# Kernel tuning notes

Hardware: AMD Instinct MI355X
Metric: run time of the kernel (lower is better)

The kernel has to match this reference:

```python
import jax, jax.numpy as jnp
import numpy as np


def setup_inputs() -> dict:
    key = jax.random.key(0)
    k = jax.random.split(key, 6)
    N, Cin, H, W = 16, 256, 14, 14   # ROI mask features
    D = 256                          # dim_reduced
    C = 20                           # number of FALKON classifiers (num_classes - 1)
    M = 512                          # max Nystrom centers (padded)
    x = jax.random.normal(k[0], (N, Cin, H, W), jnp.float32)
    # torch ConvTranspose2d weight layout: [in, out, kH, kW]
    conv_w = jax.random.normal(k[1], (Cin, D, 2, 2), jnp.float32) * 0.05
    conv_b = jnp.zeros((D,), jnp.float32)
    mean = jax.random.normal(k[2], (D,), jnp.float32) * 0.1
    mean_norm = jnp.full((1,), 10.0, jnp.float32)
    ny = jax.random.normal(k[3], (C, M, D), jnp.float32)
    alpha = jax.random.normal(k[4], (C, M, 1), jnp.float32) * 0.01
    sigma = jnp.full((1,), 25.0, jnp.float32)
    return {"x": x, "conv_w": conv_w, "conv_b": conv_b, "mean": mean,
            "mean_norm": mean_norm, "ny": ny, "alpha": alpha, "sigma": sigma}


def reference(x, conv_w, conv_b, mean, mean_norm, ny, alpha, sigma):
    N, Cin, H, W = x.shape
    D = conv_w.shape[1]
    C = ny.shape[0]
    # ConvTranspose2d(kernel=2, stride=2, pad=0): each input pixel expands to a 2x2 block.
    y = jnp.einsum('nchw,coij->nohiwj', x, conv_w).reshape(N, D, 2 * H, 2 * W)
    y = jax.nn.relu(y + conv_b[None, :, None, None])
    fw = y.shape[2]                                   # feat_width = 28
    # permute(0,2,3,1).reshape(-1, D): pixel order (roi, h, w)
    f = y.transpose(0, 2, 3, 1).reshape(-1, D)        # [P, D], P = N*fw*fw
    f = (f - mean) * (20.0 / mean_norm[0])
    # Batched Gaussian kernel mmv: K[c,p,m] = exp(-||f_p - ny_cm||^2 / (2 sigma^2))
    sq = (jnp.sum(f * f, axis=-1)[None, :, None]
          + jnp.sum(ny * ny, axis=-1)[:, None, :]
          - 2.0 * jnp.einsum('pd,cmd->cpm', f, ny))   # [C, P, M]
    K = jnp.exp(-sq / (2.0 * sigma[0] ** 2))
    scores = jnp.einsum('cpm,cm->cp', K, alpha[..., 0])  # [C, P]
    P = f.shape[0]
    bg = jnp.full((P, 1), -2.0, f.dtype)              # background column of -2
    ps = jnp.concatenate([bg, scores.T], axis=1)      # [P, C+1]
    # per-ROI: [fw*fw, C+1].T.reshape(C+1, fw, fw) == reshape(N, fw, fw, C+1) -> NCHW
    out = ps.reshape(N, fw, fw, C + 1).transpose(0, 3, 1, 2)
    return out
```

## Files before the change

kernel.cpp:

```cpp
#include <hip/hip_runtime.h>

typedef __bf16 bf16_t;
typedef __bf16 bf16x8 __attribute__((ext_vector_type(8)));
typedef __bf16 bf16x4 __attribute__((ext_vector_type(4)));
typedef float  f32x4  __attribute__((ext_vector_type(4)));
typedef float  f32x16 __attribute__((ext_vector_type(16)));
typedef char   i8x16  __attribute__((ext_vector_type(16)));
typedef char   i8x4   __attribute__((ext_vector_type(4)));
typedef int    i32x4  __attribute__((ext_vector_type(4)));

#define PIX 196
#define P_  12544
#define M_  512
#define SF  12.0f
#define SN  24.0f

__device__ inline void gload_lds16(const void* g, void* l) {
  __builtin_amdgcn_global_load_lds((const __attribute__((address_space(1))) void*)g,
                                   (__attribute__((address_space(3))) void*)l,
                                   16, 0, 0);
}

__global__ __launch_bounds__(256) void k_prep(const float* __restrict__ conv_w,
                                              const float* __restrict__ x,
                                              const float* __restrict__ ny,
                                              const float* __restrict__ alpha,
                                              const float* __restrict__ sigma,
                                              bf16_t* __restrict__ wtb,
                                              bf16_t* __restrict__ xb,
                                              char* __restrict__ nys8,
                                              float* __restrict__ e_n) {
  __shared__ float xs[16][198];
  int bid = blockIdx.x, tid = threadIdx.x;
  if (bid < 2560) {
    int l = tid & 63;
    int row = bid * 4 + (tid >> 6);
    int c = row >> 9, m = row & 511;
    f32x4 v = *reinterpret_cast<const f32x4*>(ny + row * 256 + l * 4);
    i8x4 q8;
    float sq = 0.f;
#pragma unroll
    for (int i = 0; i < 4; ++i) {
      float fq = fminf(fmaxf(__builtin_rintf(v[i] * SN), -127.f), 127.f);
      q8[i] = (char)(int)fq;
      float fv = fq * (1.f / SN);
      sq += fv * fv;
    }
    int u = m >> 5, mf = (m >> 4) & 1, mc = m & 15;
    int ks = l >> 4, lg = (l >> 2) & 3, j0 = (l & 3) * 4;
    *reinterpret_cast<i8x4*>(nys8 + (c * 16 + u) * 8192 + mf * 4096 + ks * 1024 +
                             (lg * 16 + mc) * 16 + j0) = q8;
#pragma unroll
    for (int o = 1; o < 64; o <<= 1) sq += __shfl_xor(sq, o);
    if (l == 0) {
      float s = sigma[0];
      e_n[row] = __expf(-sq / (2.f * s * s)) * alpha[row];
    }
  } else if (bid < 2816) {
    int c = bid - 2560, d = tid;
    f32x4 w = *reinterpret_cast<const f32x4*>(conv_w + (c * 256 + d) * 4);
    int ks = c >> 4, kb = (c >> 3) & 1, j = c & 7;
#pragma unroll
    for (int q = 0; q < 4; ++q) {
      int col = q * 256 + d;
      int cf = col >> 5;
      int lfrag = kb * 32 + (col & 31);
      wtb[((cf * 16 + ks) * 64 + lfrag) * 8 + j] = (bf16_t)w[q];
    }
  } else {
    int idx2 = bid - 2816;
    int n = idx2 >> 4, c0 = (idx2 & 15) * 16;
    const float* xp = x + (n * 256 + c0) * PIX;
#pragma unroll
    for (int r = 0; r < 13; ++r) {
      int idx = r * 256 + tid;
      if (idx < 3136) xs[idx / PIX][idx % PIX] = xp[idx];
    }
    __syncthreads();
#pragma unroll
    for (int r = 0; r < 4; ++r) {
      int idx = r * 256 + tid;
      if (idx < 784) {
        int hw = idx >> 2, c4 = idx & 3;
        bf16x4 h;
#pragma unroll
        for (int i = 0; i < 4; ++i) h[i] = (bf16_t)xs[c4 * 4 + i][hw];
        *reinterpret_cast<bf16x4*>(xb + (n * PIX + hw) * 256 + c0 + c4 * 4) = h;
      }
    }
  }
}

__global__ __launch_bounds__(256) void k_convT(const bf16_t* __restrict__ xb,
                                               const bf16_t* __restrict__ wtb,
                                               const float* __restrict__ conv_b,
                                               const float* __restrict__ mean,
                                               const float* __restrict__ mean_norm,
                                               char* __restrict__ fb8) {
  __shared__ bf16_t bs[32768];
  int rb = blockIdx.x * 64, cbase = blockIdx.y * 128;
  int tid = threadIdx.x, w = tid >> 6, l = tid & 63;
  int wr = w >> 1, wc = w & 1;
  const bf16_t* bsrc = wtb + blockIdx.y * 32768;
#pragma unroll
  for (int r = 0; r < 16; ++r) {
    int s = (r * 4 + w) * 64 + l;
    gload_lds16(bsrc + s * 8, bs + s * 8);
  }
  bf16x8 a[16];
  {
    const bf16_t* ap = xb + (rb + wr * 32 + (l & 31)) * 256 + (l >> 5) * 8;
#pragma unroll
    for (int ks = 0; ks < 16; ++ks) a[ks] = *reinterpret_cast<const bf16x8*>(ap + ks * 16);
  }
  __syncthreads();
  float scale = (20.f / mean_norm[0]) * SF;
  int hi = l >> 5;
#pragma unroll
  for (int cf = 0; cf < 2; ++cf) {
    f32x16 acc = {0.f,0.f,0.f,0.f,0.f,0.f,0.f,0.f,0.f,0.f,0.f,0.f,0.f,0.f,0.f,0.f};
#pragma unroll
    for (int ks = 0; ks < 16; ++ks) {
      bf16x8 b = *reinterpret_cast<const bf16x8*>(bs + ((wc * 2 + cf) * 16 + ks) * 512 + l * 8);
      acc = __builtin_amdgcn_mfma_f32_32x32x16_bf16(a[ks], b, acc, 0, 0, 0);
    }
    int col = cbase + wc * 64 + cf * 32 + (l & 31);
    int q = col >> 8, d = col & 255;
    float bias = conv_b[d], mn = mean[d];
    int qi = q >> 1, qj = q & 1;
#pragma unroll
    for (int r = 0; r < 16; ++r) {
      int p3 = rb + wr * 32 + (r & 3) + 8 * (r >> 2) + 4 * hi;
      int n = p3 / PIX, hw = p3 % PIX;
      int h = hw / 14, ww = hw % 14;
      int p = n * 784 + (2 * h + qi) * 28 + 2 * ww + qj;
      float v = fmaxf(acc[r] + bias, 0.f);
      float fq = fminf(fmaxf(__builtin_rintf((v - mn) * scale), -127.f), 127.f);
      fb8[p * 256 + d] = (char)(int)fq;
    }
  }
}

__global__ __launch_bounds__(256, 4) void k_falkon(const char* __restrict__ fb8,
                                                   const char* __restrict__ nys8,
                                                   const float* __restrict__ e_n,
                                                   const float* __restrict__ sigma,
                                                   float* __restrict__ out) {
  __shared__ char bs[2][8192];
  __shared__ float lds_en[512];
  int c = blockIdx.y, pb = blockIdx.x * 128;
  int tid = threadIdx.x, w = tid >> 6, l = tid & 63;

  if (c == 0 && tid < 128) {
    int p = pb + tid;
    out[(p / 784) * 16464 + (p % 784)] = -2.0f;
  }

  lds_en[tid] = e_n[c * M_ + tid];
  lds_en[256 + tid] = e_n[c * M_ + 256 + tid];

  i32x4 a[2][4];
  {
    const char* ap = fb8 + (pb + w * 32 + (l & 15)) * 256 + (l >> 4) * 16;
#pragma unroll
    for (int rf = 0; rf < 2; ++rf)
#pragma unroll
      for (int ks = 0; ks < 4; ++ks)
        a[rf][ks] = *reinterpret_cast<const i32x4*>(ap + rf * 16 * 256 + ks * 64);
  }

  float sg = sigma[0];
  float kl = 1.44269504088896340736f / (sg * sg);
  float Ksc = kl * (1.f / (SF * SN));

  float ef0, ef1;
#pragma unroll
  for (int rf = 0; rf < 2; ++rf) {
    int ssi = 0;
#pragma unroll
    for (int ks = 0; ks < 4; ++ks) {
      i8x16 q = __builtin_bit_cast(i8x16, a[rf][ks]);
#pragma unroll
      for (int j = 0; j < 16; ++j) {
        int qv = (signed char)q[j];
        ssi += qv * qv;
      }
    }
    ssi += __shfl_xor(ssi, 16);
    ssi += __shfl_xor(ssi, 32);
    float ef = __builtin_amdgcn_exp2f(-(float)ssi * (0.5f * kl / (SF * SF)));
    if (rf == 0) ef0 = ef; else ef1 = ef;
  }

  f32x4 sacc[2];
  sacc[0] = {0.f, 0.f, 0.f, 0.f};
  sacc[1] = {0.f, 0.f, 0.f, 0.f};

  const char* nb = nys8 + c * (16 * 8192);

  auto stage = [&](int u) {
    const char* src = nb + u * 8192;
    char* dst = &bs[u & 1][0];
#pragma unroll
    for (int r = 0; r < 2; ++r) {
      int slot = r * 256 + tid;
      gload_lds16(src + slot * 16, dst + slot * 16);
    }
  };

  stage(0);
  stage(1);
  asm volatile("s_waitcnt vmcnt(2) lgkmcnt(0)" ::: "memory");
  __builtin_amdgcn_s_barrier();

  for (int u = 0; u < 16; ++u) {
    const char* bp = &bs[u & 1][0] + l * 16;
    i32x4 b[2][4];
#pragma unroll
    for (int mf = 0; mf < 2; ++mf)
#pragma unroll
      for (int ks = 0; ks < 4; ++ks)
        b[mf][ks] = *reinterpret_cast<const i32x4*>(bp + mf * 4096 + ks * 1024);

    i32x4 acc[2][2];
#pragma unroll
    for (int rf = 0; rf < 2; ++rf)
#pragma unroll
      for (int mf = 0; mf < 2; ++mf) acc[rf][mf] = {0, 0, 0, 0};

    __builtin_amdgcn_s_setprio(1);
#pragma unroll
    for (int ks = 0; ks < 4; ++ks)
#pragma unroll
      for (int rf = 0; rf < 2; ++rf)
#pragma unroll
        for (int mf = 0; mf < 2; ++mf)
          acc[rf][mf] = __builtin_amdgcn_mfma_i32_16x16x64_i8(a[rf][ks], b[mf][ks],
                                                              acc[rf][mf], 0, 0, 0);
    __builtin_amdgcn_s_setprio(0);

    float en0 = lds_en[u * 32 + (l & 15)];
    float en1 = lds_en[u * 32 + 16 + (l & 15)];
#pragma unroll
    for (int rf = 0; rf < 2; ++rf)
#pragma unroll
      for (int r = 0; r < 4; ++r) {
        sacc[rf][r] += en0 * __builtin_amdgcn_exp2f((float)acc[rf][0][r] * Ksc)
                     + en1 * __builtin_amdgcn_exp2f((float)acc[rf][1][r] * Ksc);
      }

    if (u < 15) {
      asm volatile("s_waitcnt lgkmcnt(0)" ::: "memory");
      __builtin_amdgcn_s_barrier();
      if (u + 2 < 16) {
        stage(u + 2);
        asm volatile("s_waitcnt vmcnt(2)" ::: "memory");
      } else {
        asm volatile("s_waitcnt vmcnt(0)" ::: "memory");
      }
      __builtin_amdgcn_s_barrier();
    }
  }

#pragma unroll
  for (int rf = 0; rf < 2; ++rf)
#pragma unroll
    for (int r = 0; r < 4; ++r) {
      float v = sacc[rf][r];
      v += __shfl_xor(v, 1);
      v += __shfl_xor(v, 2);
      v += __shfl_xor(v, 4);
      v += __shfl_xor(v, 8);
      int rr = (l >> 4) * 4 + r;
      float ef = __shfl(rf == 0 ? ef0 : ef1, rr);
      if ((l & 15) == 0) {
        int p = pb + w * 32 + rf * 16 + rr;
        out[(p / 784) * 16464 + (c + 1) * 784 + (p % 784)] = v * ef;
      }
    }
}

extern "C" void kernel_launch(void* const* d_in, const int* in_sizes, int n_in,
                              void* d_out, int out_size, void* d_ws, size_t ws_size,
                              hipStream_t stream) {
  const float* x         = (const float*)d_in[0];
  const float* conv_w    = (const float*)d_in[1];
  const float* conv_b    = (const float*)d_in[2];
  const float* mean      = (const float*)d_in[3];
  const float* mean_norm = (const float*)d_in[4];
  const float* ny        = (const float*)d_in[5];
  const float* alpha     = (const float*)d_in[6];
  const float* sigma     = (const float*)d_in[7];
  float* out = (float*)d_out;

  char* ws = (char*)d_ws;
  bf16_t* wtb  = (bf16_t*)ws;
  bf16_t* xb   = (bf16_t*)(ws + 524288);
  char*   fb8  = (char*)(ws + 2129920);
  char*   nys8 = (char*)(ws + 5341184);
  float*  e_n  = (float*)(ws + 7962624);

  k_prep<<<dim3(3072), dim3(256), 0, stream>>>(conv_w, x, ny, alpha, sigma,
                                               wtb, xb, nys8, e_n);
  k_convT<<<dim3(49, 8), dim3(256), 0, stream>>>(xb, wtb, conv_b, mean, mean_norm, fb8);
  k_falkon<<<dim3(98, 20), dim3(256), 0, stream>>>(fb8, nys8, e_n, sigma, out);
}
```

Measured before the change: 66.17 us.

## Software-pipeline MFMA of next tile with exp epilogue of previous tile

```diff
diff --git a/kernel.cpp b/kernel.cpp
--- a/kernel.cpp
+++ b/kernel.cpp
@@ -141,7 +141,7 @@
   }
 }
 
-__global__ __launch_bounds__(256, 4) void k_falkon(const char* __restrict__ fb8,
+__global__ __launch_bounds__(256, 3) void k_falkon(const char* __restrict__ fb8,
                                                    const char* __restrict__ nys8,
                                                    const float* __restrict__ e_n,
                                                    const float* __restrict__ sigma,
@@ -208,58 +208,82 @@
     }
   };
 
+  i32x4 bA[2][4], bB[2][4], accA[2][2], accB[2][2];
+
+  auto loadB0 = [&](i32x4 (&b)[2][4]) {
+    const char* bp = &bs[0][0] + l * 16;
+#pragma unroll
+    for (int mf = 0; mf < 2; ++mf)
+#pragma unroll
+      for (int ks = 0; ks < 4; ++ks)
+        b[mf][ks] = *reinterpret_cast<const i32x4*>(bp + mf * 4096 + ks * 1024);
+  };
+  auto loadB1 = [&](i32x4 (&b)[2][4]) {
+    const char* bp = &bs[1][0] + l * 16;
+#pragma unroll
+    for (int mf = 0; mf < 2; ++mf)
+#pragma unroll
+      for (int ks = 0; ks < 4; ++ks)
+        b[mf][ks] = *reinterpret_cast<const i32x4*>(bp + mf * 4096 + ks * 1024);
+  };
+  auto mfmaC = [&](const i32x4 (&b)[2][4], i32x4 (&acc)[2][2]) {
+#pragma unroll
+    for (int rf = 0; rf < 2; ++rf)
+#pragma unroll
+      for (int mf = 0; mf < 2; ++mf) acc[rf][mf] = {0, 0, 0, 0};
+    __builtin_amdgcn_s_setprio(1);
+#pragma unroll
+    for (int ks = 0; ks < 4; ++ks)
+#pragma unroll
+      for (int rf = 0; rf < 2; ++rf)
+#pragma unroll
+        for (int mf = 0; mf < 2; ++mf)
+          acc[rf][mf] = __builtin_amdgcn_mfma_i32_16x16x64_i8(a[rf][ks], b[mf][ks],
+                                                              acc[rf][mf], 0, 0, 0);
+    __builtin_amdgcn_s_setprio(0);
+  };
+  auto expS = [&](int u, const i32x4 (&acc)[2][2]) {
+    float en0 = lds_en[u * 32 + (l & 15)];
+    float en1 = lds_en[u * 32 + 16 + (l & 15)];
+#pragma unroll
+    for (int rf = 0; rf < 2; ++rf)
+#pragma unroll
+      for (int r = 0; r < 4; ++r) {
+        sacc[rf][r] += en0 * __builtin_amdgcn_exp2f((float)acc[rf][0][r] * Ksc)
+                     + en1 * __builtin_amdgcn_exp2f((float)acc[rf][1][r] * Ksc);
+      }
+  };
+  auto handoff = [&](int u) {
+    asm volatile("s_waitcnt lgkmcnt(0)" ::: "memory");
+    __builtin_amdgcn_s_barrier();
+    if (u + 2 < 16) {
+      stage(u + 2);
+      asm volatile("s_waitcnt vmcnt(2)" ::: "memory");
+    } else {
+      asm volatile("s_waitcnt vmcnt(0)" ::: "memory");
+    }
+    __builtin_amdgcn_s_barrier();
+  };
+
   stage(0);
   stage(1);
   asm volatile("s_waitcnt vmcnt(2) lgkmcnt(0)" ::: "memory");
   __builtin_amdgcn_s_barrier();
 
-  for (int u = 0; u < 16; ++u) {
-    const char* bp = &bs[u & 1][0] + l * 16;
-    i32x4 b[2][4];
-#pragma unroll
-    for (int mf = 0; mf < 2; ++mf)
-#pragma unroll
-      for (int ks = 0; ks < 4; ++ks)
-        b[mf][ks] = *reinterpret_cast<const i32x4*>(bp + mf * 4096 + ks * 1024);
-
-    i32x4 acc[2][2];
-#pragma unroll
-    for (int rf = 0; rf < 2; ++rf)
-#pragma unroll
-      for (int mf = 0; mf < 2; ++mf) acc[rf][mf] = {0, 0, 0, 0};
-
-    __builtin_amdgcn_s_setprio(1);
-#pragma unroll
-    for (int ks = 0; ks < 4; ++ks)
-#pragma unroll
-      for (int rf = 0; rf < 2; ++rf)
-#pragma unroll
-        for (int mf = 0; mf < 2; ++mf)
-          acc[rf][mf] = __builtin_amdgcn_mfma_i32_16x16x64_i8(a[rf][ks], b[mf][ks],
-                                                              acc[rf][mf], 0, 0, 0);
-    __builtin_amdgcn_s_setprio(0);
-
-    float en0 = lds_en[u * 32 + (l & 15)];
-    float en1 = lds_en[u * 32 + 16 + (l & 15)];
-#pragma unroll
-    for (int rf = 0; rf < 2; ++rf)
-#pragma unroll
-      for (int r = 0; r < 4; ++r) {
-        sacc[rf][r] += en0 * __builtin_amdgcn_exp2f((float)acc[rf][0][r] * Ksc)
-                     + en1 * __builtin_amdgcn_exp2f((float)acc[rf][1][r] * Ksc);
-      }
-
-    if (u < 15) {
-      asm volatile("s_waitcnt lgkmcnt(0)" ::: "memory");
-      __builtin_amdgcn_s_barrier();
-      if (u + 2 < 16) {
-        stage(u + 2);
-        asm volatile("s_waitcnt vmcnt(2)" ::: "memory");
-      } else {
-        asm volatile("s_waitcnt vmcnt(0)" ::: "memory");
-      }
-      __builtin_amdgcn_s_barrier();
-    }
+  loadB0(bA);
+  mfmaC(bA, accA);
+  for (int t = 0; t < 8; ++t) {
+    int u = 2 * t;
+    handoff(u);
+    loadB1(bB);
+    mfmaC(bB, accB);
+    expS(u, accA);
+    if (u + 2 < 16) {
+      handoff(u + 1);
+      loadB0(bA);
+      mfmaC(bA, accA);
+    }
+    expS(u + 1, accB);
   }
 
 #pragma unroll
```

Result: slower. 70.54 us (+6.6%).

## Split Nystrom centers across waves with per-wave staging and LDS reduction

Applied to the files above, without the earlier changes.

```diff
diff --git a/kernel.cpp b/kernel.cpp
--- a/kernel.cpp
+++ b/kernel.cpp
@@ -141,17 +141,19 @@
   }
 }
 
-__global__ __launch_bounds__(256, 4) void k_falkon(const char* __restrict__ fb8,
+__global__ __launch_bounds__(256, 2) void k_falkon(const char* __restrict__ fb8,
                                                    const char* __restrict__ nys8,
                                                    const float* __restrict__ e_n,
                                                    const float* __restrict__ sigma,
                                                    float* __restrict__ out) {
-  __shared__ char bs[2][8192];
+  __shared__ char bs[4][2][8192];
   __shared__ float lds_en[512];
-  int c = blockIdx.y, pb = blockIdx.x * 128;
+  __shared__ float part[4][64];
+  __shared__ float ef_l[64];
+  int c = blockIdx.y, pb = blockIdx.x * 64;
   int tid = threadIdx.x, w = tid >> 6, l = tid & 63;
 
-  if (c == 0 && tid < 128) {
+  if (c == 0 && tid < 64) {
     int p = pb + tid;
     out[(p / 784) * 16464 + (p % 784)] = -2.0f;
   }
@@ -159,11 +161,11 @@
   lds_en[tid] = e_n[c * M_ + tid];
   lds_en[256 + tid] = e_n[c * M_ + 256 + tid];
 
-  i32x4 a[2][4];
+  i32x4 a[4][4];
   {
-    const char* ap = fb8 + (pb + w * 32 + (l & 15)) * 256 + (l >> 4) * 16;
-#pragma unroll
-    for (int rf = 0; rf < 2; ++rf)
+    const char* ap = fb8 + (pb + (l & 15)) * 256 + (l >> 4) * 16;
+#pragma unroll
+    for (int rf = 0; rf < 4; ++rf)
 #pragma unroll
       for (int ks = 0; ks < 4; ++ks)
         a[rf][ks] = *reinterpret_cast<const i32x4*>(ap + rf * 16 * 256 + ks * 64);
@@ -173,9 +175,8 @@
   float kl = 1.44269504088896340736f / (sg * sg);
   float Ksc = kl * (1.f / (SF * SN));
 
-  float ef0, ef1;
-#pragma unroll
-  for (int rf = 0; rf < 2; ++rf) {
+#pragma unroll
+  for (int rf = 0; rf < 4; ++rf) {
     int ssi = 0;
 #pragma unroll
     for (int ks = 0; ks < 4; ++ks) {
@@ -188,43 +189,42 @@
     }
     ssi += __shfl_xor(ssi, 16);
     ssi += __shfl_xor(ssi, 32);
-    float ef = __builtin_amdgcn_exp2f(-(float)ssi * (0.5f * kl / (SF * SF)));
-    if (rf == 0) ef0 = ef; else ef1 = ef;
-  }
-
-  f32x4 sacc[2];
-  sacc[0] = {0.f, 0.f, 0.f, 0.f};
-  sacc[1] = {0.f, 0.f, 0.f, 0.f};
-
-  const char* nb = nys8 + c * (16 * 8192);
+    if (w == 0 && l < 16)
+      ef_l[rf * 16 + l] = __builtin_amdgcn_exp2f(-(float)ssi * (0.5f * kl / (SF * SF)));
+  }
+
+  f32x4 sacc[4];
+#pragma unroll
+  for (int rf = 0; rf < 4; ++rf) sacc[rf] = {0.f, 0.f, 0.f, 0.f};
+
+  const char* nb = nys8 + (c * 16 + w * 4) * 8192;
 
   auto stage = [&](int u) {
     const char* src = nb + u * 8192;
-    char* dst = &bs[u & 1][0];
-#pragma unroll
-    for (int r = 0; r < 2; ++r) {
-      int slot = r * 256 + tid;
-      gload_lds16(src + slot * 16, dst + slot * 16);
-    }
+    char* dst = &bs[w][u & 1][0];
+#pragma unroll
+    for (int r = 0; r < 8; ++r)
+      gload_lds16(src + (r * 64 + l) * 16, dst + (r * 64 + l) * 16);
   };
 
   stage(0);
   stage(1);
-  asm volatile("s_waitcnt vmcnt(2) lgkmcnt(0)" ::: "memory");
-  __builtin_amdgcn_s_barrier();
-
-  for (int u = 0; u < 16; ++u) {
-    const char* bp = &bs[u & 1][0] + l * 16;
+  __syncthreads();
+
+  for (int u = 0; u < 4; ++u) {
+    const char* bp = &bs[w][u & 1][0] + l * 16;
     i32x4 b[2][4];
 #pragma unroll
     for (int mf = 0; mf < 2; ++mf)
 #pragma unroll
       for (int ks = 0; ks < 4; ++ks)
         b[mf][ks] = *reinterpret_cast<const i32x4*>(bp + mf * 4096 + ks * 1024);
-
-    i32x4 acc[2][2];
-#pragma unroll
-    for (int rf = 0; rf < 2; ++rf)
+    asm volatile("s_waitcnt lgkmcnt(0)" ::: "memory");
+    if (u + 2 < 4) stage(u + 2);
+
+    i32x4 acc[4][2];
+#pragma unroll
+    for (int rf = 0; rf < 4; ++rf)
 #pragma unroll
       for (int mf = 0; mf < 2; ++mf) acc[rf][mf] = {0, 0, 0, 0};
 
@@ -232,38 +232,32 @@
 #pragma unroll
     for (int ks = 0; ks < 4; ++ks)
 #pragma unroll
-      for (int rf = 0; rf < 2; ++rf)
+      for (int rf = 0; rf < 4; ++rf)
 #pragma unroll
         for (int mf = 0; mf < 2; ++mf)
           acc[rf][mf] = __builtin_amdgcn_mfma_i32_16x16x64_i8(a[rf][ks], b[mf][ks],
                                                               acc[rf][mf], 0, 0, 0);
     __builtin_amdgcn_s_setprio(0);
 
-    float en0 = lds_en[u * 32 + (l & 15)];
-    float en1 = lds_en[u * 32 + 16 + (l & 15)];
-#pragma unroll
-    for (int rf = 0; rf < 2; ++rf)
+    float en0 = lds_en[w * 128 + u * 32 + (l & 15)];
+    float en1 = lds_en[w * 128 + u * 32 + 16 + (l & 15)];
+#pragma unroll
+    for (int rf = 0; rf < 4; ++rf)
 #pragma unroll
       for (int r = 0; r < 4; ++r) {
         sacc[rf][r] += en0 * __builtin_amdgcn_exp2f((float)acc[rf][0][r] * Ksc)
                      + en1 * __builtin_amdgcn_exp2f((float)acc[rf][1][r] * Ksc);
       }
 
-    if (u < 15) {
-      asm volatile("s_waitcnt lgkmcnt(0)" ::: "memory");
-      __builtin_amdgcn_s_barrier();
-      if (u + 2 < 16) {
-        stage(u + 2);
-        asm volatile("s_waitcnt vmcnt(2)" ::: "memory");
-      } else {
-        asm volatile("s_waitcnt vmcnt(0)" ::: "memory");
-      }
-      __builtin_amdgcn_s_barrier();
-    }
-  }
-
-#pragma unroll
-  for (int rf = 0; rf < 2; ++rf)
+    if (u == 1) {
+      asm volatile("s_waitcnt vmcnt(8)" ::: "memory");
+    } else if (u == 2) {
+      asm volatile("s_waitcnt vmcnt(0)" ::: "memory");
+    }
+  }
+
+#pragma unroll
+  for (int rf = 0; rf < 4; ++rf)
 #pragma unroll
     for (int r = 0; r < 4; ++r) {
       float v = sacc[rf][r];
@@ -271,13 +265,15 @@
       v += __shfl_xor(v, 2);
       v += __shfl_xor(v, 4);
       v += __shfl_xor(v, 8);
-      int rr = (l >> 4) * 4 + r;
-      float ef = __shfl(rf == 0 ? ef0 : ef1, rr);
-      if ((l & 15) == 0) {
-        int p = pb + w * 32 + rf * 16 + rr;
-        out[(p / 784) * 16464 + (c + 1) * 784 + (p % 784)] = v * ef;
-      }
-    }
+      if ((l & 15) == 0) part[w][rf * 16 + (l >> 4) * 4 + r] = v;
+    }
+  __syncthreads();
+
+  if (tid < 64) {
+    float s = part[0][tid] + part[1][tid] + part[2][tid] + part[3][tid];
+    int p = pb + tid;
+    out[(p / 784) * 16464 + (c + 1) * 784 + (p % 784)] = s * ef_l[tid];
+  }
 }
 
 extern "C" void kernel_launch(void* const* d_in, const int* in_sizes, int n_in,
@@ -303,5 +299,5 @@
   k_prep<<<dim3(3072), dim3(256), 0, stream>>>(conv_w, x, ny, alpha, sigma,
                                                wtb, xb, nys8, e_n);
   k_convT<<<dim3(49, 8), dim3(256), 0, stream>>>(xb, wtb, conv_b, mean, mean_norm, fb8);
-  k_falkon<<<dim3(98, 20), dim3(256), 0, stream>>>(fb8, nys8, e_n, sigma, out);
-}
+  k_falkon<<<dim3(196, 20), dim3(256), 0, stream>>>(fb8, nys8, e_n, sigma, out);
+}
```

After: 104.3 us. +57.6%, slower.
